# Kernel optimization log

Measured on AMD Instinct MI355X. Metric: run time of the kernel, lower is better.

Reference implementation:

```python
import jax, jax.numpy as jnp
import numpy as np

V, D, MAXLEN, B, C = 32000, 1024, 2048, 4, 2048


def setup_inputs() -> dict:
    key = jax.random.key(0)
    ks = jax.random.split(key, 8)
    x = jax.random.randint(ks[0], (B, C), 0, V, dtype=jnp.int64)
    s = 0.02
    embed = jax.random.normal(ks[1], (V, D), dtype=jnp.float32) * s
    pe = jax.random.normal(ks[2], (MAXLEN, D), dtype=jnp.float32) * s
    Wq = jax.random.normal(ks[3], (D, D), dtype=jnp.float32) * s
    Wk = jax.random.normal(ks[4], (D, D), dtype=jnp.float32) * s
    Wv = jax.random.normal(ks[5], (D, D), dtype=jnp.float32) * s
    Wo = jax.random.normal(ks[6], (V, D), dtype=jnp.float32) * s
    bo = jnp.zeros((V,), dtype=jnp.float32)
    return {"x": x, "embed": embed, "pe": pe, "Wq": Wq, "Wk": Wk, "Wv": Wv, "Wo": Wo, "bo": bo}


def reference(x, embed, pe, Wq, Wk, Wv, Wo, bo):
    Bc, Cc = x.shape
    Dd = embed.shape[1]
    # token embedding + learned absolute PE (pos_offset = 0)
    h = embed[x] + pe[:Cc]                      # (B, C, D)
    # single-head Q/K/V projections (torch Linear: y = x @ W.T)
    Q = jnp.einsum('bcd,ed->bce', h, Wq)
    K = jnp.einsum('bcd,ed->bce', h, Wk)
    Vv = jnp.einsum('bcd,ed->bce', h, Wv)
    scores = jnp.einsum('bqd,bkd->bqk', Q, K) / jnp.sqrt(jnp.float32(Dd))
    # additive causal mask: 0 on lower triangle, -inf above
    mask = jnp.where(jnp.tril(jnp.ones((Cc, Cc), dtype=bool)), 0.0, -jnp.inf).astype(scores.dtype)
    weights = jax.nn.softmax(scores + mask, axis=-1)  # (B, C, C)
    attn_out = jnp.einsum('bqk,bkd->bqd', weights, Vv)
    hidden = h + attn_out
    logits = jnp.einsum('bcd,vd->bcv', hidden, Wo) + bo
    return logits
```

## Files before the change

### kernel.cpp

```cpp
#include <hip/hip_runtime.h>

#define DEV __device__ __forceinline__

typedef __attribute__((ext_vector_type(8))) __bf16 bf16x8;
typedef __attribute__((ext_vector_type(4))) float f32x4;

DEV unsigned short f2bf(float f) {
    unsigned u = __builtin_bit_cast(unsigned, f);
    u += 0x7fffu + ((u >> 16) & 1u);
    return (unsigned short)(u >> 16);
}
DEV float bf2f(unsigned short s) {
    unsigned u = ((unsigned)s) << 16;
    return __builtin_bit_cast(float, u);
}

DEV void gload_lds16(const unsigned short* g, unsigned short* l) {
    __builtin_amdgcn_global_load_lds(
        (const __attribute__((address_space(1))) unsigned int*)g,
        (__attribute__((address_space(3))) unsigned int*)l, 16, 0, 0);
}


__global__ __launch_bounds__(256) void k_cast_bf16(const float* __restrict__ src,
                                                   unsigned short* __restrict__ dst, int n4) {
    int i = blockIdx.x * 256 + threadIdx.x;
    if (i >= n4) return;
    float4 v = reinterpret_cast<const float4*>(src)[i];
    ushort4 o;
    o.x = f2bf(v.x); o.y = f2bf(v.y); o.z = f2bf(v.z); o.w = f2bf(v.w);
    reinterpret_cast<ushort4*>(dst)[i] = o;
}

__global__ __launch_bounds__(256) void k_prep_h(const int* __restrict__ x,
                                                const float* __restrict__ embed,
                                                const float* __restrict__ pe,
                                                unsigned short* __restrict__ h) {
    const int r = blockIdx.x;
    const int pos = r & 2047;
    const int tok = x[r];
    const int t = threadIdx.x;
    float4 e = reinterpret_cast<const float4*>(embed + (size_t)tok * 1024)[t];
    float4 p = reinterpret_cast<const float4*>(pe + (size_t)pos * 1024)[t];
    ushort4 o;
    o.x = f2bf(e.x + p.x); o.y = f2bf(e.y + p.y);
    o.z = f2bf(e.z + p.z); o.w = f2bf(e.w + p.w);
    reinterpret_cast<ushort4*>(h + (size_t)r * 1024)[t] = o;
}

__global__ __launch_bounds__(256) void k_softmax_causal(const float* __restrict__ S,
                                                        unsigned short* __restrict__ W) {
    const int r = blockIdx.x;
    const int q = r & 2047;
    const float* row = S + (size_t)r * 2048;
    unsigned short* orow = W + (size_t)r * 2048;
    const int t = threadIdx.x;
    const float scale = 0.03125f;
    float p[8];
    float mx = -1e30f;
    #pragma unroll
    for (int i = 0; i < 2; ++i) {
        int i4 = t + i * 256;
        float4 v = reinterpret_cast<const float4*>(row)[i4];
        int base = i4 * 4;
        p[i*4+0] = (base+0 <= q) ? v.x * scale : -1e30f;
        p[i*4+1] = (base+1 <= q) ? v.y * scale : -1e30f;
        p[i*4+2] = (base+2 <= q) ? v.z * scale : -1e30f;
        p[i*4+3] = (base+3 <= q) ? v.w * scale : -1e30f;
        #pragma unroll
        for (int j = 0; j < 4; ++j) mx = fmaxf(mx, p[i*4+j]);
    }
    #pragma unroll
    for (int o = 32; o > 0; o >>= 1) mx = fmaxf(mx, __shfl_xor(mx, o));
    __shared__ float redm[4];
    __shared__ float reds[4];
    const int w = t >> 6;
    if ((t & 63) == 0) redm[w] = mx;
    __syncthreads();
    mx = fmaxf(fmaxf(redm[0], redm[1]), fmaxf(redm[2], redm[3]));
    float e[8];
    float s = 0.f;
    #pragma unroll
    for (int i = 0; i < 8; ++i) { e[i] = __expf(p[i] - mx); s += e[i]; }
    #pragma unroll
    for (int o = 32; o > 0; o >>= 1) s += __shfl_xor(s, o);
    if ((t & 63) == 0) reds[w] = s;
    __syncthreads();
    s = (reds[0] + reds[1]) + (reds[2] + reds[3]);
    const float inv = 1.0f / s;
    #pragma unroll
    for (int i = 0; i < 2; ++i) {
        int i4 = t + i * 256;
        ushort4 o4;
        o4.x = f2bf(e[i*4+0] * inv);
        o4.y = f2bf(e[i*4+1] * inv);
        o4.z = f2bf(e[i*4+2] * inv);
        o4.w = f2bf(e[i*4+3] * inv);
        reinterpret_cast<ushort4*>(orow)[i4] = o4;
    }
}

template<int OUT_BF16, int TRANS_OUT, int ADD_BIAS, int ADD_RES, int CAUSAL_SKIP, int TRI_K>
__global__ __launch_bounds__(256)
void k_gemm_bt(const unsigned short* __restrict__ A,
               const unsigned short* __restrict__ B,
               void* __restrict__ Out,
               const float* __restrict__ bias,
               const unsigned short* __restrict__ Res,
               int M, int N, int K, int ldo,
               long long sA, long long sB, long long sC, long long sRes) {
    const int bm = blockIdx.x, bn = blockIdx.y, bz = blockIdx.z;
    if (CAUSAL_SKIP && bn > bm) return;
    A += (long long)bz * sA;
    B += (long long)bz * sB;

    __shared__ __align__(16) unsigned short As[128 * 32];
    __shared__ __align__(16) unsigned short Bs[128 * 32];

    const int t = threadIdx.x;
    const int w = t >> 6;
    const int lane = t & 63;
    const int wm = w >> 1, wn = w & 1;
    const int fr = lane & 15, fq = lane >> 4;

    f32x4 acc[4][4];
    #pragma unroll
    for (int mi = 0; mi < 4; ++mi)
        #pragma unroll
        for (int ni = 0; ni < 4; ++ni)
            acc[mi][ni] = (f32x4){0.f, 0.f, 0.f, 0.f};

    const int kend = TRI_K ? ((K < (bm + 1) * 128) ? K : (bm + 1) * 128) : K;

    const int c0 = t, c1 = t + 256;
    const unsigned short* gA0 = A + (size_t)(bm * 128 + (c0 >> 2)) * K + (c0 & 3) * 8;
    const unsigned short* gA1 = A + (size_t)(bm * 128 + (c1 >> 2)) * K + (c1 & 3) * 8;
    const unsigned short* gB0 = B + (size_t)(bn * 128 + (c0 >> 2)) * K + (c0 & 3) * 8;
    const unsigned short* gB1 = B + (size_t)(bn * 128 + (c1 >> 2)) * K + (c1 & 3) * 8;
    unsigned short* lA0 = As + w * 512;
    unsigned short* lA1 = As + 2048 + w * 512;
    unsigned short* lB0 = Bs + w * 512;
    unsigned short* lB1 = Bs + 2048 + w * 512;

    for (int kt = 0; kt < kend; kt += 32) {
        gload_lds16(gA0 + kt, lA0);
        gload_lds16(gA1 + kt, lA1);
        gload_lds16(gB0 + kt, lB0);
        gload_lds16(gB1 + kt, lB1);
        __syncthreads();

        bf16x8 af[4], bfr[4];
        #pragma unroll
        for (int mi = 0; mi < 4; ++mi)
            af[mi] = *reinterpret_cast<const bf16x8*>(As + (wm * 64 + mi * 16 + fr) * 32 + fq * 8);
        #pragma unroll
        for (int ni = 0; ni < 4; ++ni)
            bfr[ni] = *reinterpret_cast<const bf16x8*>(Bs + (wn * 64 + ni * 16 + fr) * 32 + fq * 8);
        #pragma unroll
        for (int mi = 0; mi < 4; ++mi)
            #pragma unroll
            for (int ni = 0; ni < 4; ++ni)
                acc[mi][ni] = __builtin_amdgcn_mfma_f32_16x16x32_bf16(af[mi], bfr[ni], acc[mi][ni], 0, 0, 0);
        __syncthreads();
    }

    const int row0 = bm * 128 + wm * 64 + fq * 4;
    const int col0 = bn * 128 + wn * 64 + fr;
    if (OUT_BF16 && TRANS_OUT) {
        unsigned short* O = (unsigned short*)Out + (long long)bz * sC;
        #pragma unroll
        for (int mi = 0; mi < 4; ++mi) {
            const int rr = row0 + mi * 16;
            #pragma unroll
            for (int ni = 0; ni < 4; ++ni) {
                const int col = col0 + ni * 16;
                ushort4 o4;
                o4.x = f2bf(acc[mi][ni][0]);
                o4.y = f2bf(acc[mi][ni][1]);
                o4.z = f2bf(acc[mi][ni][2]);
                o4.w = f2bf(acc[mi][ni][3]);
                *reinterpret_cast<ushort4*>(O + (size_t)col * ldo + rr) = o4;
            }
        }
    } else if (OUT_BF16) {
        unsigned short* O = (unsigned short*)Out + (long long)bz * sC;
        #pragma unroll
        for (int mi = 0; mi < 4; ++mi) {
            #pragma unroll
            for (int j = 0; j < 4; ++j) {
                const int row = row0 + mi * 16 + j;
                unsigned short* orow = O + (size_t)row * ldo;
                const unsigned short* rrow =
                    ADD_RES ? (Res + (long long)bz * sRes + (size_t)row * ldo) : (const unsigned short*)nullptr;
                #pragma unroll
                for (int ni = 0; ni < 4; ++ni) {
                    const int col = col0 + ni * 16;
                    float v = acc[mi][ni][j];
                    if (ADD_RES) v += bf2f(rrow[col]);
                    orow[col] = f2bf(v);
                }
            }
        }
    } else {
        float* O = (float*)Out + (long long)bz * sC;
        #pragma unroll
        for (int mi = 0; mi < 4; ++mi) {
            #pragma unroll
            for (int j = 0; j < 4; ++j) {
                const int row = row0 + mi * 16 + j;
                float* orow = O + (size_t)row * ldo;
                #pragma unroll
                for (int ni = 0; ni < 4; ++ni) {
                    const int col = col0 + ni * 16;
                    float v = acc[mi][ni][j];
                    if (ADD_BIAS) v += bias[col];
                    orow[col] = v;
                }
            }
        }
    }
}


#define RGN(buf, op, kk) (((((buf)*2+(op))*2)+(kk))*8192)

#define STG_A(buf, kk, kt) do { \
    unsigned short* d_ = Lds + RGN(buf,0,kk) + w*512; \
    gload_lds16(gA0 + (kt)*64 + (kk)*32, d_); \
    gload_lds16(gA1 + (kt)*64 + (kk)*32, d_ + 4096); } while(0)

#define STG_B(buf, kk, kt) do { \
    unsigned short* d_ = Lds + RGN(buf,1,kk) + w*512; \
    gload_lds16(gB0 + (kt)*64 + (kk)*32, d_); \
    gload_lds16(gB1 + (kt)*64 + (kk)*32, d_ + 4096); } while(0)

#define PH(buf, kk, mh, LOADB, STG, VM) do { \
    if (LOADB) { \
        _Pragma("unroll") \
        for (int ni_ = 0; ni_ < 4; ++ni_) \
            bfrag[ni_] = *reinterpret_cast<const bf16x8*>(Lds + RGN(buf,1,kk) + bBase + ni_*512); \
    } \
    bf16x8 afrag[4]; \
    _Pragma("unroll") \
    for (int j_ = 0; j_ < 4; ++j_) \
        afrag[j_] = *reinterpret_cast<const bf16x8*>(Lds + RGN(buf,0,kk) + aBase + ((mh)*4+j_)*512); \
    STG; \
    asm volatile("s_barrier" ::: "memory"); \
    asm volatile("s_waitcnt lgkmcnt(0)" ::: "memory"); \
    __builtin_amdgcn_sched_barrier(0); \
    __builtin_amdgcn_s_setprio(1); \
    _Pragma("unroll") \
    for (int j_ = 0; j_ < 4; ++j_) \
        _Pragma("unroll") \
        for (int ni_ = 0; ni_ < 4; ++ni_) \
            acc[(mh)*4+j_][ni_] = __builtin_amdgcn_mfma_f32_16x16x32_bf16(afrag[j_], bfrag[ni_], acc[(mh)*4+j_][ni_], 0, 0, 0); \
    __builtin_amdgcn_s_setprio(0); \
    __builtin_amdgcn_sched_barrier(0); \
    if (VM) asm volatile("s_waitcnt vmcnt(8)" ::: "memory"); \
    asm volatile("s_barrier" ::: "memory"); \
} while(0)

__global__ __launch_bounds__(512, 2)
void k_gemm256_bias(const unsigned short* __restrict__ A,
                    const unsigned short* __restrict__ B,
                    float* __restrict__ Out,
                    const float* __restrict__ bias,
                    int N, int K) {
    __shared__ __align__(16) unsigned short Lds[65536];

    int wg = blockIdx.x;
    const int cpx = gridDim.x >> 3;
    wg = (wg & 7) * cpx + (wg >> 3);
    const int t = wg / 20, u = wg % 20;
    const int tm = t & 7, tn = t >> 3;
    const int bm = tm * 4 + (u & 3);
    const int bn = tn * 5 + (u >> 2);

    const int tid = threadIdx.x;
    const int w = tid >> 6, lane = tid & 63;
    const int wm = w >> 2, wn = w & 3;
    const int fr = lane & 15, fq = lane >> 4;
    const int sl = fq ^ ((fr >> 1) & 3);
    const int nt = K >> 6;
    const int m_ = nt - 1;

    const int c0 = w * 64 + lane, c1 = c0 + 512;
    const int r0 = c0 >> 2, s0 = ((c0 & 3) ^ ((r0 >> 1) & 3)) * 8;
    const int r1 = c1 >> 2, s1 = ((c1 & 3) ^ ((r1 >> 1) & 3)) * 8;
    const unsigned short* gA0 = A + (size_t)(bm * 256 + r0) * K + s0;
    const unsigned short* gA1 = A + (size_t)(bm * 256 + r1) * K + s1;
    const unsigned short* gB0 = B + (size_t)(bn * 256 + r0) * K + s0;
    const unsigned short* gB1 = B + (size_t)(bn * 256 + r1) * K + s1;

    const int aBase = (wm * 128 + fr) * 32 + sl * 8;
    const int bBase = (wn * 64 + fr) * 32 + sl * 8;

    f32x4 acc[8][4];
    #pragma unroll
    for (int i = 0; i < 8; ++i)
        #pragma unroll
        for (int j = 0; j < 4; ++j)
            acc[i][j] = (f32x4){0.f, 0.f, 0.f, 0.f};
    bf16x8 bfrag[4];

    STG_A(0,0,0); STG_B(0,0,0);
    STG_A(0,1,0); STG_B(0,1,0);
    STG_A(1,0,1); STG_B(1,0,1);
    asm volatile("s_waitcnt vmcnt(8)" ::: "memory");
    asm volatile("s_barrier" ::: "memory");

    for (int tt = 0; tt < nt; tt += 2) {
        const int tp1 = (tt + 1) & m_, tp2 = (tt + 2) & m_, tp3 = (tt + 3) & m_;
        PH(0, 0, 0, 1, STG_A(1,1,tp1), 0);
        PH(0, 0, 1, 0, STG_B(1,1,tp1), 1);
        PH(0, 1, 0, 1, STG_A(0,0,tp2), 0);
        PH(0, 1, 1, 0, STG_B(0,0,tp2), 1);
        PH(1, 0, 0, 1, STG_A(0,1,tp2), 0);
        PH(1, 0, 1, 0, STG_B(0,1,tp2), 1);
        PH(1, 1, 0, 1, STG_A(1,0,tp3), 0);
        PH(1, 1, 1, 0, STG_B(1,0,tp3), 1);
    }

    const int row0 = bm * 256 + wm * 128 + fq * 4;
    const int col0 = bn * 256 + wn * 64 + fr;
    float bia[4];
    #pragma unroll
    for (int ni = 0; ni < 4; ++ni) bia[ni] = bias[col0 + ni * 16];
    #pragma unroll
    for (int mi = 0; mi < 8; ++mi) {
        #pragma unroll
        for (int j = 0; j < 4; ++j) {
            const int row = row0 + mi * 16 + j;
            float* orow = Out + (size_t)row * N;
            #pragma unroll
            for (int ni = 0; ni < 4; ++ni)
                orow[col0 + ni * 16] = acc[mi][ni][j] + bia[ni];
        }
    }
    asm volatile("s_waitcnt vmcnt(0)" ::: "memory");
}


extern "C" void kernel_launch(void* const* d_in, const int* in_sizes, int n_in,
                              void* d_out, int out_size, void* d_ws, size_t ws_size,
                              hipStream_t stream) {
    (void)in_sizes; (void)n_in; (void)out_size; (void)ws_size;
    constexpr int Bb = 4, Cc = 2048, Dd = 1024, Vv = 32000;
    constexpr int M = Bb * Cc;

    const int*   x     = (const int*)d_in[0];
    const float* embed = (const float*)d_in[1];
    const float* pe    = (const float*)d_in[2];
    const float* Wq    = (const float*)d_in[3];
    const float* Wk    = (const float*)d_in[4];
    const float* Wv    = (const float*)d_in[5];
    const float* Wo    = (const float*)d_in[6];
    const float* bo    = (const float*)d_in[7];
    float* out = (float*)d_out;

    char* p = (char*)d_ws;
    auto au = [&](size_t n) { unsigned short* r = (unsigned short*)p; p += n * sizeof(unsigned short); return r; };
    unsigned short* h_bf   = au((size_t)M * Dd);
    unsigned short* hid_bf = au((size_t)M * Dd);
    unsigned short* Qb     = au((size_t)M * Dd);
    unsigned short* Kb     = au((size_t)M * Dd);
    unsigned short* Vt     = au((size_t)M * Dd);
    unsigned short* Wqb    = au((size_t)Dd * Dd);
    unsigned short* Wkb    = au((size_t)Dd * Dd);
    unsigned short* Wvb    = au((size_t)Dd * Dd);
    unsigned short* Wob    = au((size_t)Vv * Dd);
    unsigned short* Wt     = au((size_t)Bb * Cc * Cc);
    float* Sc = (float*)p;

    k_cast_bf16<<<dim3(Dd * Dd / 4 / 256), 256, 0, stream>>>(Wq, Wqb, Dd * Dd / 4);
    k_cast_bf16<<<dim3(Dd * Dd / 4 / 256), 256, 0, stream>>>(Wk, Wkb, Dd * Dd / 4);
    k_cast_bf16<<<dim3(Dd * Dd / 4 / 256), 256, 0, stream>>>(Wv, Wvb, Dd * Dd / 4);
    k_cast_bf16<<<dim3(Vv * Dd / 4 / 256), 256, 0, stream>>>(Wo, Wob, Vv * Dd / 4);
    k_prep_h<<<dim3(M), 256, 0, stream>>>(x, embed, pe, h_bf);

    {
        dim3 g(M / 128, Dd / 128, 1);
        k_gemm_bt<1,0,0,0,0,0><<<g, 256, 0, stream>>>(h_bf, Wqb, Qb, nullptr, nullptr,
            M, Dd, Dd, Dd, 0, 0, 0, 0);
        k_gemm_bt<1,0,0,0,0,0><<<g, 256, 0, stream>>>(h_bf, Wkb, Kb, nullptr, nullptr,
            M, Dd, Dd, Dd, 0, 0, 0, 0);
    }
    {
        dim3 g(Cc / 128, Dd / 128, Bb);
        k_gemm_bt<1,1,0,0,0,0><<<g, 256, 0, stream>>>(h_bf, Wvb, Vt, nullptr, nullptr,
            Cc, Dd, Dd, Cc, (long long)Cc * Dd, 0, (long long)Dd * Cc, 0);
    }
    {
        dim3 g(Cc / 128, Cc / 128, Bb);
        k_gemm_bt<0,0,0,0,1,0><<<g, 256, 0, stream>>>(Qb, Kb, Sc, nullptr, nullptr,
            Cc, Cc, Dd, Cc, (long long)Cc * Dd, (long long)Cc * Dd, (long long)Cc * Cc, 0);
    }
    k_softmax_causal<<<dim3(M), 256, 0, stream>>>(Sc, Wt);
    {
        dim3 g(Cc / 128, Dd / 128, Bb);
        k_gemm_bt<1,0,0,1,0,1><<<g, 256, 0, stream>>>(Wt, Vt, hid_bf, nullptr, h_bf,
            Cc, Dd, Cc, Dd, (long long)Cc * Cc, (long long)Dd * Cc, (long long)Cc * Dd, (long long)Cc * Dd);
    }
    {
        const int gm = M / 256;
        const int gn = Vv / 256;
        k_gemm256_bias<<<dim3(gm * gn), 512, 0, stream>>>(hid_bf, Wob, out, bo, Vv, Dd);
    }
}
```

Baseline: 856.0 us.

## Make output GEMM persistent over four M tiles, trim causal softmax loads, fuse casts

The big vocab GEMM now launches 1000 workgroups, and each loops over four consecutive 256-row M tiles for one N tile. The software pipeline keeps running across tile boundaries by prefetching the next tile's first K slices, and bias loads are hoisted. This is meant to cut tail and launch imbalance and the per-tile prologue cost, in exchange for longer-lived blocks and fewer concurrent tiles. The causal softmax skips loading masked score chunks and only writes up to the 128-aligned causal limit. The three QKV weight casts are merged into a single launch.

```diff
diff --git a/kernel.cpp b/kernel.cpp
--- a/kernel.cpp
+++ b/kernel.cpp
@@ -30,6 +30,23 @@
     ushort4 o;
     o.x = f2bf(v.x); o.y = f2bf(v.y); o.z = f2bf(v.z); o.w = f2bf(v.w);
     reinterpret_cast<ushort4*>(dst)[i] = o;
+}
+
+__global__ __launch_bounds__(256) void k_cast3(const float* __restrict__ a,
+                                               const float* __restrict__ b,
+                                               const float* __restrict__ c,
+                                               unsigned short* __restrict__ oa,
+                                               unsigned short* __restrict__ ob,
+                                               unsigned short* __restrict__ oc,
+                                               int n4each) {
+    int i = blockIdx.x * 256 + threadIdx.x;
+    int w = i / n4each, j = i - w * n4each;
+    const float* s = (w == 0) ? a : (w == 1) ? b : c;
+    unsigned short* d = (w == 0) ? oa : (w == 1) ? ob : oc;
+    float4 v = reinterpret_cast<const float4*>(s)[j];
+    ushort4 o;
+    o.x = f2bf(v.x); o.y = f2bf(v.y); o.z = f2bf(v.z); o.w = f2bf(v.w);
+    reinterpret_cast<ushort4*>(d)[j] = o;
 }
 
 __global__ __launch_bounds__(256) void k_prep_h(const int* __restrict__ x,
@@ -56,13 +73,15 @@
     unsigned short* orow = W + (size_t)r * 2048;
     const int t = threadIdx.x;
     const float scale = 0.03125f;
+    const int kceil4 = (((q >> 7) + 1) << 7) >> 2;
     float p[8];
     float mx = -1e30f;
     #pragma unroll
     for (int i = 0; i < 2; ++i) {
         int i4 = t + i * 256;
-        float4 v = reinterpret_cast<const float4*>(row)[i4];
         int base = i4 * 4;
+        float4 v = (float4){0.f, 0.f, 0.f, 0.f};
+        if (base <= q) v = reinterpret_cast<const float4*>(row)[i4];
         p[i*4+0] = (base+0 <= q) ? v.x * scale : -1e30f;
         p[i*4+1] = (base+1 <= q) ? v.y * scale : -1e30f;
         p[i*4+2] = (base+2 <= q) ? v.z * scale : -1e30f;
@@ -91,12 +110,14 @@
     #pragma unroll
     for (int i = 0; i < 2; ++i) {
         int i4 = t + i * 256;
-        ushort4 o4;
-        o4.x = f2bf(e[i*4+0] * inv);
-        o4.y = f2bf(e[i*4+1] * inv);
-        o4.z = f2bf(e[i*4+2] * inv);
-        o4.w = f2bf(e[i*4+3] * inv);
-        reinterpret_cast<ushort4*>(orow)[i4] = o4;
+        if (i4 < kceil4) {
+            ushort4 o4;
+            o4.x = f2bf(e[i*4+0] * inv);
+            o4.y = f2bf(e[i*4+1] * inv);
+            o4.z = f2bf(e[i*4+2] * inv);
+            o4.w = f2bf(e[i*4+3] * inv);
+            reinterpret_cast<ushort4*>(orow)[i4] = o4;
+        }
     }
 }
 
@@ -228,6 +249,11 @@
     unsigned short* d_ = Lds + RGN(buf,0,kk) + w*512; \
     gload_lds16(gA0 + (kt)*64 + (kk)*32, d_); \
     gload_lds16(gA1 + (kt)*64 + (kk)*32, d_ + 4096); } while(0)
+
+#define STG_An(buf, kk, kt) do { \
+    unsigned short* d_ = Lds + RGN(buf,0,kk) + w*512; \
+    gload_lds16(gA0n + (kt)*64 + (kk)*32, d_); \
+    gload_lds16(gA1n + (kt)*64 + (kk)*32, d_ + 4096); } while(0)
 
 #define STG_B(buf, kk, kt) do { \
     unsigned short* d_ = Lds + RGN(buf,1,kk) + w*512; \
@@ -261,34 +287,31 @@
 } while(0)
 
 __global__ __launch_bounds__(512, 2)
-void k_gemm256_bias(const unsigned short* __restrict__ A,
-                    const unsigned short* __restrict__ B,
-                    float* __restrict__ Out,
-                    const float* __restrict__ bias,
-                    int N, int K) {
+void k_gemm256_bias_p(const unsigned short* __restrict__ A,
+                      const unsigned short* __restrict__ B,
+                      float* __restrict__ Out,
+                      const float* __restrict__ bias,
+                      int N, int K) {
     __shared__ __align__(16) unsigned short Lds[65536];
 
     int wg = blockIdx.x;
     const int cpx = gridDim.x >> 3;
     wg = (wg & 7) * cpx + (wg >> 3);
-    const int t = wg / 20, u = wg % 20;
-    const int tm = t & 7, tn = t >> 3;
-    const int bm = tm * 4 + (u & 3);
-    const int bn = tn * 5 + (u >> 2);
+    const int bq = wg & 7;
+    const int bn = wg >> 3;
 
     const int tid = threadIdx.x;
     const int w = tid >> 6, lane = tid & 63;
     const int wm = w >> 2, wn = w & 3;
     const int fr = lane & 15, fq = lane >> 4;
     const int sl = fq ^ ((fr >> 1) & 3);
-    const int nt = K >> 6;
-    const int m_ = nt - 1;
 
     const int c0 = w * 64 + lane, c1 = c0 + 512;
     const int r0 = c0 >> 2, s0 = ((c0 & 3) ^ ((r0 >> 1) & 3)) * 8;
     const int r1 = c1 >> 2, s1 = ((c1 & 3) ^ ((r1 >> 1) & 3)) * 8;
-    const unsigned short* gA0 = A + (size_t)(bm * 256 + r0) * K + s0;
-    const unsigned short* gA1 = A + (size_t)(bm * 256 + r1) * K + s1;
+    const long long segStride = (long long)256 * K;
+    const unsigned short* gA0 = A + (size_t)(bq * 1024 + r0) * K + s0;
+    const unsigned short* gA1 = A + (size_t)(bq * 1024 + r1) * K + s1;
     const unsigned short* gB0 = B + (size_t)(bn * 256 + r0) * K + s0;
     const unsigned short* gB1 = B + (size_t)(bn * 256 + r1) * K + s1;
 
@@ -302,6 +325,11 @@
         for (int j = 0; j < 4; ++j)
             acc[i][j] = (f32x4){0.f, 0.f, 0.f, 0.f};
     bf16x8 bfrag[4];
+
+    const int col0 = bn * 256 + wn * 64 + fr;
+    float bia[4];
+    #pragma unroll
+    for (int ni = 0; ni < 4; ++ni) bia[ni] = bias[col0 + ni * 16];
 
     STG_A(0,0,0); STG_B(0,0,0);
     STG_A(0,1,0); STG_B(0,1,0);
@@ -309,33 +337,49 @@
     asm volatile("s_waitcnt vmcnt(8)" ::: "memory");
     asm volatile("s_barrier" ::: "memory");
 
-    for (int tt = 0; tt < nt; tt += 2) {
-        const int tp1 = (tt + 1) & m_, tp2 = (tt + 2) & m_, tp3 = (tt + 3) & m_;
-        PH(0, 0, 0, 1, STG_A(1,1,tp1), 0);
-        PH(0, 0, 1, 0, STG_B(1,1,tp1), 1);
-        PH(0, 1, 0, 1, STG_A(0,0,tp2), 0);
-        PH(0, 1, 1, 0, STG_B(0,0,tp2), 1);
-        PH(1, 0, 0, 1, STG_A(0,1,tp2), 0);
-        PH(1, 0, 1, 0, STG_B(0,1,tp2), 1);
-        PH(1, 1, 0, 1, STG_A(1,0,tp3), 0);
-        PH(1, 1, 1, 0, STG_B(1,0,tp3), 1);
-    }
-
-    const int row0 = bm * 256 + wm * 128 + fq * 4;
-    const int col0 = bn * 256 + wn * 64 + fr;
-    float bia[4];
-    #pragma unroll
-    for (int ni = 0; ni < 4; ++ni) bia[ni] = bias[col0 + ni * 16];
-    #pragma unroll
-    for (int mi = 0; mi < 8; ++mi) {
-        #pragma unroll
-        for (int j = 0; j < 4; ++j) {
-            const int row = row0 + mi * 16 + j;
-            float* orow = Out + (size_t)row * N;
-            #pragma unroll
-            for (int ni = 0; ni < 4; ++ni)
-                orow[col0 + ni * 16] = acc[mi][ni][j] + bia[ni];
-        }
+    for (int s = 0; s < 4; ++s) {
+        const unsigned short* gA0n = (s < 3) ? gA0 + segStride : gA0;
+        const unsigned short* gA1n = (s < 3) ? gA1 + segStride : gA1;
+
+        for (int tt = 0; tt < 14; tt += 2) {
+            const int tp1 = tt + 1, tp2 = tt + 2, tp3 = tt + 3;
+            PH(0, 0, 0, 1, STG_A(1,1,tp1), 0);
+            PH(0, 0, 1, 0, STG_B(1,1,tp1), 1);
+            PH(0, 1, 0, 1, STG_A(0,0,tp2), 0);
+            PH(0, 1, 1, 0, STG_B(0,0,tp2), 1);
+            PH(1, 0, 0, 1, STG_A(0,1,tp2), 0);
+            PH(1, 0, 1, 0, STG_B(0,1,tp2), 1);
+            PH(1, 1, 0, 1, STG_A(1,0,tp3), 0);
+            PH(1, 1, 1, 0, STG_B(1,0,tp3), 1);
+        }
+        PH(0, 0, 0, 1, STG_A(1,1,15), 0);
+        PH(0, 0, 1, 0, STG_B(1,1,15), 1);
+        PH(0, 1, 0, 1, STG_An(0,0,0), 0);
+        PH(0, 1, 1, 0, STG_B(0,0,0), 1);
+        PH(1, 0, 0, 1, STG_An(0,1,0), 0);
+        PH(1, 0, 1, 0, STG_B(0,1,0), 1);
+        PH(1, 1, 0, 1, STG_An(1,0,1), 0);
+        PH(1, 1, 1, 0, STG_B(1,0,1), 1);
+
+        const int row0 = (bq * 4 + s) * 256 + wm * 128 + fq * 4;
+        #pragma unroll
+        for (int mi = 0; mi < 8; ++mi) {
+            #pragma unroll
+            for (int j = 0; j < 4; ++j) {
+                const int row = row0 + mi * 16 + j;
+                float* orow = Out + (size_t)row * N;
+                #pragma unroll
+                for (int ni = 0; ni < 4; ++ni)
+                    orow[col0 + ni * 16] = acc[mi][ni][j] + bia[ni];
+            }
+        }
+        #pragma unroll
+        for (int i = 0; i < 8; ++i)
+            #pragma unroll
+            for (int j = 0; j < 4; ++j)
+                acc[i][j] = (f32x4){0.f, 0.f, 0.f, 0.f};
+
+        gA0 = gA0n; gA1 = gA1n;
     }
     asm volatile("s_waitcnt vmcnt(0)" ::: "memory");
 }
@@ -372,9 +416,7 @@
     unsigned short* Wt     = au((size_t)Bb * Cc * Cc);
     float* Sc = (float*)p;
 
-    k_cast_bf16<<<dim3(Dd * Dd / 4 / 256), 256, 0, stream>>>(Wq, Wqb, Dd * Dd / 4);
-    k_cast_bf16<<<dim3(Dd * Dd / 4 / 256), 256, 0, stream>>>(Wk, Wkb, Dd * Dd / 4);
-    k_cast_bf16<<<dim3(Dd * Dd / 4 / 256), 256, 0, stream>>>(Wv, Wvb, Dd * Dd / 4);
+    k_cast3<<<dim3(3 * Dd * Dd / 4 / 256), 256, 0, stream>>>(Wq, Wk, Wv, Wqb, Wkb, Wvb, Dd * Dd / 4);
     k_cast_bf16<<<dim3(Vv * Dd / 4 / 256), 256, 0, stream>>>(Wo, Wob, Vv * Dd / 4);
     k_prep_h<<<dim3(M), 256, 0, stream>>>(x, embed, pe, h_bf);
 
@@ -401,9 +443,5 @@
         k_gemm_bt<1,0,0,1,0,1><<<g, 256, 0, stream>>>(Wt, Vt, hid_bf, nullptr, h_bf,
             Cc, Dd, Cc, Dd, (long long)Cc * Cc, (long long)Dd * Cc, (long long)Cc * Dd, (long long)Cc * Dd);
     }
-    {
-        const int gm = M / 256;
-        const int gn = Vv / 256;
-        k_gemm256_bias<<<dim3(gm * gn), 512, 0, stream>>>(hid_bf, Wob, out, bo, Vv, Dd);
-    }
-}
+    k_gemm256_bias_p<<<dim3(1000), 512, 0, stream>>>(hid_bf, Wob, out, bo, Vv, Dd);
+}
```

New measurement: 829.5 us. 3.1% less time.
